# Kernel optimization log

Measured on AMD Instinct MI355X. Metric: run time of the kernel, lower is better.

## Reference

```python
import jax, jax.numpy as jnp
import numpy as np

N, EM, EW, L, S = 20000, 100000, 25000, 128, 6


def _mlp(x, W1, b1, W2, b2, g, beta):
    # Linear -> ReLU -> Linear -> LayerNorm
    h = jax.nn.relu(x @ W1 + b1) @ W2 + b2
    mu = jnp.mean(h, axis=-1, keepdims=True)
    var = jnp.mean((h - mu) ** 2, axis=-1, keepdims=True)
    return g * (h - mu) * jax.lax.rsqrt(var + 1e-5) + beta


def _scatter_mean(attr, recv, n):
    s = jax.ops.segment_sum(attr, recv, num_segments=n)
    c = jax.ops.segment_sum(jnp.ones((attr.shape[0], 1), attr.dtype), recv, num_segments=n)
    return s / jnp.maximum(c, 1.0)


def setup_inputs() -> dict:
    key = jax.random.key(0)
    ks = jax.random.split(key, 16)

    def w(k, shape, fan_in):
        return (jax.random.normal(k, shape, jnp.float32) / np.sqrt(fan_in).astype(np.float32))

    inp = {
        'x': jax.random.normal(ks[0], (N, L), jnp.float32),
        'mesh_edge_attr': jax.random.normal(ks[1], (EM, L), jnp.float32),
        'world_edge_attr': jax.random.normal(ks[2], (EW, L), jnp.float32),
        'mesh_edge_index': jax.random.randint(ks[3], (2, EM), 0, N),
        'world_edge_index': jax.random.randint(ks[4], (2, EW), 0, N),
    }
    i = 5
    for pre in ('me', 'we', 'nd'):
        inp[pre + '_W1'] = w(ks[i], (S, 3 * L, L), 3 * L); i += 1
        inp[pre + '_b1'] = jnp.zeros((S, L), jnp.float32)
        inp[pre + '_W2'] = w(ks[i], (S, L, L), L); i += 1
        inp[pre + '_b2'] = jnp.zeros((S, L), jnp.float32)
        inp[pre + '_g'] = jnp.ones((S, L), jnp.float32)
        inp[pre + '_beta'] = jnp.zeros((S, L), jnp.float32)
    return inp


def reference(x, mesh_edge_attr, world_edge_attr, mesh_edge_index, world_edge_index,
              me_W1, me_b1, me_W2, me_b2, me_g, me_beta,
              we_W1, we_b1, we_W2, we_b2, we_g, we_beta,
              nd_W1, nd_b1, nd_W2, nd_b2, nd_g, nd_beta):
    ms, mr = mesh_edge_index[0], mesh_edge_index[1]
    ws, wr = world_edge_index[0], world_edge_index[1]
    n = x.shape[0]

    def step(carry, p):
        x, mea, wea = carry
        (mW1, mb1, mW2, mb2, mg, mbe,
         wW1, wb1, wW2, wb2, wg, wbe,
         nW1, nb1, nW2, nb2, ng, nbe) = p
        # EdgeModel: gather + concat + MLP, residual into edge attrs
        mea = mea + _mlp(jnp.concatenate([x[ms], x[mr], mea], axis=-1), mW1, mb1, mW2, mb2, mg, mbe)
        wea = wea + _mlp(jnp.concatenate([x[ws], x[wr], wea], axis=-1), wW1, wb1, wW2, wb2, wg, wbe)
        # NodeModel: scatter-mean over both edge sets + concat + MLP, residual
        agg = jnp.concatenate([x, _scatter_mean(mea, mr, n), _scatter_mean(wea, wr, n)], axis=-1)
        x = x + _mlp(agg, nW1, nb1, nW2, nb2, ng, nbe)
        return (x, mea, wea), None

    params = (me_W1, me_b1, me_W2, me_b2, me_g, me_beta,
              we_W1, we_b1, we_W2, we_b2, we_g, we_beta,
              nd_W1, nd_b1, nd_W2, nd_b2, nd_g, nd_beta)
    (x, mea, wea), _ = jax.lax.scan(step, (x, mesh_edge_attr, world_edge_attr), params)
    return x, mea, wea
```

## Files before the change

### kernel.cpp

```cpp
#include <hip/hip_runtime.h>

constexpr int LDIM  = 128;
constexpr int NNODE = 20000;
constexpr int EM_N  = 100000;
constexpr int EW_N  = 25000;
constexpr int NSTEP = 6;

typedef short bf16x8 __attribute__((ext_vector_type(8)));
typedef short bf16x4 __attribute__((ext_vector_type(4)));
typedef float f32x4  __attribute__((ext_vector_type(4)));

struct MlpParams {
  const float* x;
  const float* attrIn;
  float*       attrOut;
  const int*   src;
  const int*   dst;
  float*       sum1;
  float*       sum2;
  const float* inv1;
  const float* inv2;
  const short* W1H;
  const short* W2H;
  const short* W2L;
  const float* b1;
  const float* b2;
  const float* gam;
  const float* bet;
  int nRows;
};

__device__ __forceinline__ short f2b(float f) {
  unsigned int u = __float_as_uint(f);
  u = (u + 0x7fffu + ((u >> 16) & 1u)) >> 16;
  return (short)u;
}
__device__ __forceinline__ float b2f(short s) {
  return __uint_as_float(((unsigned int)(unsigned short)s) << 16);
}
__device__ __forceinline__ bf16x4 cvt4(float4 a, float sc) {
  bf16x4 o;
  o[0] = f2b(a.x * sc); o[1] = f2b(a.y * sc);
  o[2] = f2b(a.z * sc); o[3] = f2b(a.w * sc);
  return o;
}

template<bool IS_EDGE>
__launch_bounds__(256, 2)
__global__ void mlp_kernel(MlpParams pmA, MlpParams pmB, int blocksA) {
  const bool isA = (int)blockIdx.x < blocksA;
  const MlpParams P = isA ? pmA : pmB;
  const int bid  = isA ? (int)blockIdx.x : (int)blockIdx.x - blocksA;
  const int row0 = bid * 128;

  __shared__ __align__(16) short Abuf[128][40];
  __shared__ __align__(16) short Bhi[128][40];
  __shared__ __align__(16) short Blo[128][40];
  __shared__ __align__(16) short Hbuf[128][136];
  __shared__ float b1s[128], b2s[128], gs[128], bes[128];
  __shared__ int   idxa[128], idxb[128];
  __shared__ float inv1s[128], inv2s[128];
  __shared__ float sumL[2][128], sqL[2][128];
  __shared__ float muL[128], rsL[128];

  const int t = threadIdx.x;

  if (t < 128) {
    b1s[t] = P.b1[t];
    gs[t]  = P.gam[t];
    if (IS_EDGE) {
      int r = row0 + t;
      idxa[t] = (r < P.nRows) ? P.src[r] : 0;
    } else {
      int r = min(row0 + t, P.nRows - 1);
      inv1s[t] = P.inv1[r];
    }
  } else {
    int t2 = t - 128;
    b2s[t2] = P.b2[t2];
    bes[t2] = P.bet[t2];
    if (IS_EDGE) {
      int r = row0 + t2;
      idxb[t2] = (r < P.nRows) ? P.dst[r] : 0;
    } else {
      int r = min(row0 + t2, P.nRows - 1);
      inv2s[t2] = P.inv2[r];
    }
  }
  __syncthreads();

  const int l   = t & 63;
  const int wid = t >> 6;
  const int wr  = wid >> 1, wcc = wid & 1;
  const int lr  = l & 15,  lg  = l >> 4;

  const int  srow  = t >> 1, sh = t & 1;
  const int  sgRow = row0 + srow;
  const bool sval  = sgRow < P.nRows;
  const int  sgC   = sval ? sgRow : 0;
  const float vmask = sval ? 1.f : 0.f;

  const float* base0; const float* base1; const float* base2;
  float sc1v = vmask, sc2v = vmask;
  if (IS_EDGE) {
    base0 = P.x + (size_t)idxa[srow] * LDIM + sh * 16;
    base1 = P.x + (size_t)idxb[srow] * LDIM + sh * 16;
    base2 = P.attrIn + (size_t)sgC * LDIM + sh * 16;
  } else {
    base0 = P.x    + (size_t)sgC * LDIM + sh * 16;
    base1 = P.sum1 + (size_t)sgC * LDIM + sh * 16;
    base2 = P.sum2 + (size_t)sgC * LDIM + sh * 16;
    sc1v = inv1s[srow] * vmask;
    sc2v = inv2s[srow] * vmask;
  }

  const int wrow = t >> 1, wsh = t & 1;
  const short* w1base = P.W1H + (size_t)wrow * 384 + wsh * 16;

  f32x4 acc[4][4];
#pragma unroll
  for (int i = 0; i < 4; ++i)
#pragma unroll
    for (int j = 0; j < 4; ++j) acc[i][j] = f32x4{0.f, 0.f, 0.f, 0.f};

  float4 pA0, pA1, pA2, pA3;
  bf16x8 pW0, pW1;
  {
    const float4* bp = (const float4*)base0;
    pA0 = bp[0]; pA1 = bp[1]; pA2 = bp[2]; pA3 = bp[3];
    pW0 = *(const bf16x8*)w1base;
    pW1 = *(const bf16x8*)(w1base + 8);
  }

#pragma unroll
  for (int kc = 0; kc < 12; ++kc) {
    const int seg = kc >> 2, part = kc & 3;
    if (kc > 0) __syncthreads();
    {
      const float scK = (seg == 0) ? vmask : (seg == 1) ? sc1v : sc2v;
      *(bf16x4*)&Abuf[srow][sh * 16 + 0]  = cvt4(pA0, scK);
      *(bf16x4*)&Abuf[srow][sh * 16 + 4]  = cvt4(pA1, scK);
      *(bf16x4*)&Abuf[srow][sh * 16 + 8]  = cvt4(pA2, scK);
      *(bf16x4*)&Abuf[srow][sh * 16 + 12] = cvt4(pA3, scK);
      *(bf16x8*)&Bhi[wrow][wsh * 16]     = pW0;
      *(bf16x8*)&Bhi[wrow][wsh * 16 + 8] = pW1;
      if constexpr (!IS_EDGE) {
        if (seg != 0 && sval) {
          float4 z = {0.f, 0.f, 0.f, 0.f};
          float4* zp = (float4*)((seg == 1 ? base1 : base2) + part * 32);
          zp[0] = z; zp[1] = z; zp[2] = z; zp[3] = z;
        }
      }
    }
    __syncthreads();
    if (kc < 11) {
      const int kn = kc + 1, segn = kn >> 2, partn = kn & 3;
      const float4* bp = (const float4*)((segn == 0 ? base0 : segn == 1 ? base1 : base2) + partn * 32);
      pA0 = bp[0]; pA1 = bp[1]; pA2 = bp[2]; pA3 = bp[3];
      pW0 = *(const bf16x8*)(w1base + kn * 32);
      pW1 = *(const bf16x8*)(w1base + kn * 32 + 8);
    }
    bf16x8 av[4], bh[4];
#pragma unroll
    for (int mi = 0; mi < 4; ++mi)
      av[mi] = *(const bf16x8*)&Abuf[wr * 64 + mi * 16 + lr][lg * 8];
#pragma unroll
    for (int ni = 0; ni < 4; ++ni)
      bh[ni] = *(const bf16x8*)&Bhi[wcc * 64 + ni * 16 + lr][lg * 8];
#pragma unroll
    for (int mi = 0; mi < 4; ++mi)
#pragma unroll
      for (int ni = 0; ni < 4; ++ni)
        acc[mi][ni] = __builtin_amdgcn_mfma_f32_16x16x32_bf16(av[mi], bh[ni], acc[mi][ni], 0, 0, 0);
  }

#pragma unroll
  for (int rt = 0; rt < 4; ++rt)
#pragma unroll
    for (int ct = 0; ct < 4; ++ct) {
      const int cc = wcc * 64 + ct * 16 + lr;
      const float bb = b1s[cc];
#pragma unroll
      for (int q = 0; q < 4; ++q) {
        const int rr = wr * 64 + rt * 16 + lg * 4 + q;
        Hbuf[rr][cc] = f2b(fmaxf(acc[rt][ct][q] + bb, 0.f));
      }
    }

  f32x4 acc2[4][4];
#pragma unroll
  for (int i = 0; i < 4; ++i)
#pragma unroll
    for (int j = 0; j < 4; ++j) acc2[i][j] = f32x4{0.f, 0.f, 0.f, 0.f};

  const short* w2hbase = P.W2H + (size_t)wrow * 128 + wsh * 16;
  const short* w2lbase = P.W2L + (size_t)wrow * 128 + wsh * 16;

  bf16x8 qh0, qh1, ql0, ql1;
  qh0 = *(const bf16x8*)w2hbase;
  qh1 = *(const bf16x8*)(w2hbase + 8);
  ql0 = *(const bf16x8*)w2lbase;
  ql1 = *(const bf16x8*)(w2lbase + 8);

#pragma unroll
  for (int kc = 0; kc < 4; ++kc) {
    __syncthreads();
    {
      *(bf16x8*)&Bhi[wrow][wsh * 16]     = qh0;
      *(bf16x8*)&Bhi[wrow][wsh * 16 + 8] = qh1;
      *(bf16x8*)&Blo[wrow][wsh * 16]     = ql0;
      *(bf16x8*)&Blo[wrow][wsh * 16 + 8] = ql1;
    }
    __syncthreads();
    if (kc < 3) {
      qh0 = *(const bf16x8*)(w2hbase + (kc + 1) * 32);
      qh1 = *(const bf16x8*)(w2hbase + (kc + 1) * 32 + 8);
      ql0 = *(const bf16x8*)(w2lbase + (kc + 1) * 32);
      ql1 = *(const bf16x8*)(w2lbase + (kc + 1) * 32 + 8);
    }
    bf16x8 av2[4], bh2[4], bl2[4];
#pragma unroll
    for (int rt = 0; rt < 4; ++rt)
      av2[rt] = *(const bf16x8*)&Hbuf[wr * 64 + rt * 16 + lr][kc * 32 + lg * 8];
#pragma unroll
    for (int ct = 0; ct < 4; ++ct) {
      bh2[ct] = *(const bf16x8*)&Bhi[wcc * 64 + ct * 16 + lr][lg * 8];
      bl2[ct] = *(const bf16x8*)&Blo[wcc * 64 + ct * 16 + lr][lg * 8];
    }
#pragma unroll
    for (int rt = 0; rt < 4; ++rt)
#pragma unroll
      for (int ct = 0; ct < 4; ++ct) {
        acc2[rt][ct] = __builtin_amdgcn_mfma_f32_16x16x32_bf16(av2[rt], bl2[ct], acc2[rt][ct], 0, 0, 0);
        acc2[rt][ct] = __builtin_amdgcn_mfma_f32_16x16x32_bf16(av2[rt], bh2[ct], acc2[rt][ct], 0, 0, 0);
      }
  }

  float s1[4][4], s2[4][4];
#pragma unroll
  for (int rt = 0; rt < 4; ++rt)
#pragma unroll
    for (int q = 0; q < 4; ++q) { s1[rt][q] = 0.f; s2[rt][q] = 0.f; }
#pragma unroll
  for (int rt = 0; rt < 4; ++rt)
#pragma unroll
    for (int ct = 0; ct < 4; ++ct) {
      const float bb = b2s[wcc * 64 + ct * 16 + lr];
#pragma unroll
      for (int q = 0; q < 4; ++q) {
        float v = acc2[rt][ct][q] + bb;
        acc2[rt][ct][q] = v;
        s1[rt][q] += v;
        s2[rt][q] += v * v;
      }
    }
#pragma unroll
  for (int m = 1; m < 16; m <<= 1) {
#pragma unroll
    for (int rt = 0; rt < 4; ++rt)
#pragma unroll
      for (int q = 0; q < 4; ++q) {
        s1[rt][q] += __shfl_xor(s1[rt][q], m);
        s2[rt][q] += __shfl_xor(s2[rt][q], m);
      }
  }
  __syncthreads();
  {
    const int rt = lr >> 2, q = lr & 3;
    const int rr = wr * 64 + rt * 16 + lg * 4 + q;
    sumL[wcc][rr] = s1[rt][q];
    sqL[wcc][rr]  = s2[rt][q];
  }
  __syncthreads();
  if (t < 128) {
    const float tot = sumL[0][t] + sumL[1][t];
    const float tsq = sqL[0][t] + sqL[1][t];
    const float mu  = tot * (1.0f / 128.0f);
    const float var = tsq * (1.0f / 128.0f) - mu * mu;
    muL[t] = mu;
    rsL[t] = rsqrtf(var + 1e-5f);
  }
  __syncthreads();

#pragma unroll
  for (int rt = 0; rt < 4; ++rt) {
#pragma unroll
    for (int q = 0; q < 4; ++q) {
      const int rr = wr * 64 + rt * 16 + lg * 4 + q;
      const int grow = row0 + rr;
      if (grow < P.nRows) {
        const float mu = muL[rr], rs = rsL[rr];
        const float* rin = P.attrIn + (size_t)grow * LDIM;
        float* rout = P.attrOut + (size_t)grow * LDIM;
        float* ssum = nullptr;
        if (IS_EDGE) ssum = P.sum1 + (size_t)idxb[rr] * LDIM;
#pragma unroll
        for (int ct = 0; ct < 4; ++ct) {
          const int cc = wcc * 64 + ct * 16 + lr;
          const float o = gs[cc] * (acc2[rt][ct][q] - mu) * rs + bes[cc] + rin[cc];
          rout[cc] = o;
          if (IS_EDGE) atomicAdd(ssum + cc, o);
        }
      }
    }
  }
}

__global__ void prep_weights(const float* w1a, const float* w1b, const float* w1c,
                             const float* w2a, const float* w2b, const float* w2c,
                             short* w1h, short* w2h, short* w2l) {
  int i = blockIdx.x * 256 + threadIdx.x;
  constexpr int N1 = 18 * 128 * 384;
  constexpr int N2 = 18 * 128 * 128;
  if (i < N1) {
    int g = i / (128 * 384);
    int rem = i - g * (128 * 384);
    int n = rem / 384, k = rem - n * 384;
    int m = g / 6, s = g - m * 6;
    const float* src = (m == 0) ? w1a : (m == 1) ? w1b : w1c;
    w1h[i] = f2b(src[(size_t)s * (384 * 128) + (size_t)k * 128 + n]);
  } else if (i < N1 + N2) {
    int j = i - N1;
    int g = j / (128 * 128);
    int rem = j - g * (128 * 128);
    int n = rem / 128, k = rem - n * 128;
    int m = g / 6, s = g - m * 6;
    const float* src = (m == 0) ? w2a : (m == 1) ? w2b : w2c;
    float f = src[(size_t)s * (128 * 128) + (size_t)k * 128 + n];
    short hi = f2b(f);
    w2h[j] = hi;
    w2l[j] = f2b(f - b2f(hi));
  }
}

__global__ void prep_deg(const int* mr, const int* wrcv, int* degm, int* degw) {
  int i = blockIdx.x * 256 + threadIdx.x;
  if (i < EM_N) atomicAdd(&degm[mr[i]], 1);
  else if (i < EM_N + EW_N) atomicAdd(&degw[wrcv[i - EM_N]], 1);
}

__global__ void prep_inv(const int* degm, const int* degw, float* invm, float* invw) {
  int i = blockIdx.x * 256 + threadIdx.x;
  if (i < NNODE) {
    invm[i] = 1.0f / fmaxf((float)degm[i], 1.0f);
    invw[i] = 1.0f / fmaxf((float)degw[i], 1.0f);
  }
}

extern "C" void kernel_launch(void* const* d_in, const int* in_sizes, int n_in,
                              void* d_out, int out_size, void* d_ws, size_t ws_size,
                              hipStream_t stream) {
  (void)in_sizes; (void)n_in; (void)out_size; (void)ws_size;
  const float* x_in   = (const float*)d_in[0];
  const float* mea_in = (const float*)d_in[1];
  const float* wea_in = (const float*)d_in[2];
  const int*   mei    = (const int*)d_in[3];
  const int*   wei    = (const int*)d_in[4];
  const float* W1s[3] = { (const float*)d_in[5],  (const float*)d_in[11], (const float*)d_in[17] };
  const float* B1s[3] = { (const float*)d_in[6],  (const float*)d_in[12], (const float*)d_in[18] };
  const float* W2s[3] = { (const float*)d_in[7],  (const float*)d_in[13], (const float*)d_in[19] };
  const float* B2s[3] = { (const float*)d_in[8],  (const float*)d_in[14], (const float*)d_in[20] };
  const float* Gs[3]  = { (const float*)d_in[9],  (const float*)d_in[15], (const float*)d_in[21] };
  const float* Be[3]  = { (const float*)d_in[10], (const float*)d_in[16], (const float*)d_in[22] };

  float* xo  = (float*)d_out;
  float* meo = xo  + (size_t)NNODE * LDIM;
  float* weo = meo + (size_t)EM_N * LDIM;

  float* msum = (float*)d_ws;
  float* wsum = msum + (size_t)NNODE * LDIM;
  int*   degm = (int*)(wsum + (size_t)NNODE * LDIM);
  int*   degw = degm + NNODE;
  float* invm = (float*)(degw + NNODE);
  float* invw = invm + NNODE;
  short* w1h  = (short*)(invw + NNODE);
  short* w2h  = w1h + (size_t)18 * 128 * 384;
  short* w2l  = w2h + (size_t)18 * 128 * 128;

  size_t zbytes = (size_t)2 * NNODE * LDIM * 4 + (size_t)2 * NNODE * 4;
  hipMemsetAsync(d_ws, 0, zbytes, stream);

  {
    int tot = 18 * 128 * 384 + 18 * 128 * 128;
    prep_weights<<<dim3((tot + 255) / 256), 256, 0, stream>>>(
        W1s[0], W1s[1], W1s[2], W2s[0], W2s[1], W2s[2], w1h, w2h, w2l);
  }
  prep_deg<<<dim3((EM_N + EW_N + 255) / 256), 256, 0, stream>>>(mei + EM_N, wei + EW_N, degm, degw);
  prep_inv<<<dim3((NNODE + 255) / 256), 256, 0, stream>>>(degm, degw, invm, invw);

  const int MB = (EM_N + 127) / 128;
  const int WB = (EW_N + 127) / 128;
  const int NB = (NNODE + 127) / 128;

  const float* xc = x_in;
  const float* mc = mea_in;
  const float* wc = wea_in;

  for (int s = 0; s < NSTEP; ++s) {
    MlpParams pm{}, pw{}, pn{};

    pm.x = xc; pm.attrIn = mc; pm.attrOut = meo;
    pm.src = mei; pm.dst = mei + EM_N;
    pm.sum1 = msum;
    pm.W1H = w1h + (size_t)(0 * 6 + s) * 128 * 384;
    pm.W2H = w2h + (size_t)(0 * 6 + s) * 128 * 128;
    pm.W2L = w2l + (size_t)(0 * 6 + s) * 128 * 128;
    pm.b1 = B1s[0] + s * LDIM; pm.b2 = B2s[0] + s * LDIM;
    pm.gam = Gs[0] + s * LDIM; pm.bet = Be[0] + s * LDIM;
    pm.nRows = EM_N;

    pw.x = xc; pw.attrIn = wc; pw.attrOut = weo;
    pw.src = wei; pw.dst = wei + EW_N;
    pw.sum1 = wsum;
    pw.W1H = w1h + (size_t)(1 * 6 + s) * 128 * 384;
    pw.W2H = w2h + (size_t)(1 * 6 + s) * 128 * 128;
    pw.W2L = w2l + (size_t)(1 * 6 + s) * 128 * 128;
    pw.b1 = B1s[1] + s * LDIM; pw.b2 = B2s[1] + s * LDIM;
    pw.gam = Gs[1] + s * LDIM; pw.bet = Be[1] + s * LDIM;
    pw.nRows = EW_N;

    mlp_kernel<true><<<dim3(MB + WB), 256, 0, stream>>>(pm, pw, MB);

    pn.x = xc; pn.attrIn = xc; pn.attrOut = xo;
    pn.sum1 = msum; pn.sum2 = wsum; pn.inv1 = invm; pn.inv2 = invw;
    pn.W1H = w1h + (size_t)(2 * 6 + s) * 128 * 384;
    pn.W2H = w2h + (size_t)(2 * 6 + s) * 128 * 128;
    pn.W2L = w2l + (size_t)(2 * 6 + s) * 128 * 128;
    pn.b1 = B1s[2] + s * LDIM; pn.b2 = B2s[2] + s * LDIM;
    pn.gam = Gs[2] + s * LDIM; pn.bet = Be[2] + s * LDIM;
    pn.nRows = NNODE;

    mlp_kernel<false><<<dim3(NB), 256, 0, stream>>>(pn, pn, NB);

    xc = xo; mc = meo; wc = weo;
  }
}
```

Before: 886.0 us.

## Drop split-bf16 W2 correction and alias A-tile into H buffer for occupancy

Removes the low-order bf16 correction term for the second-layer weights, halving the second GEMM's MFMA count and its weight traffic. The A staging tile now reuses the H buffer's shared memory, which together with the removed Blo buffer cuts LDS usage so launch bounds can ask for 3 blocks per CU. A barrier is added before H is written so the aliasing stays safe. The trade-off is lower precision in the W2 product, which may drift over the six steps.

New measurement: 919.6 us. 1.04x slower.

```diff
diff --git a/kernel.cpp b/kernel.cpp
--- a/kernel.cpp
+++ b/kernel.cpp
@@ -22,7 +22,6 @@
   const float* inv2;
   const short* W1H;
   const short* W2H;
-  const short* W2L;
   const float* b1;
   const float* b2;
   const float* gam;
@@ -46,22 +45,22 @@
 }
 
 template<bool IS_EDGE>
-__launch_bounds__(256, 2)
+__launch_bounds__(256, 3)
 __global__ void mlp_kernel(MlpParams pmA, MlpParams pmB, int blocksA) {
   const bool isA = (int)blockIdx.x < blocksA;
   const MlpParams P = isA ? pmA : pmB;
   const int bid  = isA ? (int)blockIdx.x : (int)blockIdx.x - blocksA;
   const int row0 = bid * 128;
 
-  __shared__ __align__(16) short Abuf[128][40];
+  __shared__ __align__(16) short Hbuf[128][136];
   __shared__ __align__(16) short Bhi[128][40];
-  __shared__ __align__(16) short Blo[128][40];
-  __shared__ __align__(16) short Hbuf[128][136];
   __shared__ float b1s[128], b2s[128], gs[128], bes[128];
   __shared__ int   idxa[128], idxb[128];
   __shared__ float inv1s[128], inv2s[128];
   __shared__ float sumL[2][128], sqL[2][128];
   __shared__ float muL[128], rsL[128];
+
+  short (*Abuf)[40] = (short (*)[40])(&Hbuf[0][0]);
 
   const int t = threadIdx.x;
 
@@ -174,6 +173,8 @@
         acc[mi][ni] = __builtin_amdgcn_mfma_f32_16x16x32_bf16(av[mi], bh[ni], acc[mi][ni], 0, 0, 0);
   }
 
+  __syncthreads();
+
 #pragma unroll
   for (int rt = 0; rt < 4; ++rt)
 #pragma unroll
@@ -193,47 +194,34 @@
 #pragma unroll
     for (int j = 0; j < 4; ++j) acc2[i][j] = f32x4{0.f, 0.f, 0.f, 0.f};
 
-  const short* w2hbase = P.W2H + (size_t)wrow * 128 + wsh * 16;
-  const short* w2lbase = P.W2L + (size_t)wrow * 128 + wsh * 16;
-
-  bf16x8 qh0, qh1, ql0, ql1;
-  qh0 = *(const bf16x8*)w2hbase;
-  qh1 = *(const bf16x8*)(w2hbase + 8);
-  ql0 = *(const bf16x8*)w2lbase;
-  ql1 = *(const bf16x8*)(w2lbase + 8);
+  const short* w2base = P.W2H + (size_t)wrow * 128 + wsh * 16;
+  bf16x8 q0 = *(const bf16x8*)w2base;
+  bf16x8 q1 = *(const bf16x8*)(w2base + 8);
 
 #pragma unroll
   for (int kc = 0; kc < 4; ++kc) {
     __syncthreads();
     {
-      *(bf16x8*)&Bhi[wrow][wsh * 16]     = qh0;
-      *(bf16x8*)&Bhi[wrow][wsh * 16 + 8] = qh1;
-      *(bf16x8*)&Blo[wrow][wsh * 16]     = ql0;
-      *(bf16x8*)&Blo[wrow][wsh * 16 + 8] = ql1;
+      *(bf16x8*)&Bhi[wrow][wsh * 16]     = q0;
+      *(bf16x8*)&Bhi[wrow][wsh * 16 + 8] = q1;
     }
     __syncthreads();
     if (kc < 3) {
-      qh0 = *(const bf16x8*)(w2hbase + (kc + 1) * 32);
-      qh1 = *(const bf16x8*)(w2hbase + (kc + 1) * 32 + 8);
-      ql0 = *(const bf16x8*)(w2lbase + (kc + 1) * 32);
-      ql1 = *(const bf16x8*)(w2lbase + (kc + 1) * 32 + 8);
-    }
-    bf16x8 av2[4], bh2[4], bl2[4];
+      q0 = *(const bf16x8*)(w2base + (kc + 1) * 32);
+      q1 = *(const bf16x8*)(w2base + (kc + 1) * 32 + 8);
+    }
+    bf16x8 av2[4], bh2[4];
 #pragma unroll
     for (int rt = 0; rt < 4; ++rt)
       av2[rt] = *(const bf16x8*)&Hbuf[wr * 64 + rt * 16 + lr][kc * 32 + lg * 8];
 #pragma unroll
-    for (int ct = 0; ct < 4; ++ct) {
+    for (int ct = 0; ct < 4; ++ct)
       bh2[ct] = *(const bf16x8*)&Bhi[wcc * 64 + ct * 16 + lr][lg * 8];
-      bl2[ct] = *(const bf16x8*)&Blo[wcc * 64 + ct * 16 + lr][lg * 8];
-    }
 #pragma unroll
     for (int rt = 0; rt < 4; ++rt)
 #pragma unroll
-      for (int ct = 0; ct < 4; ++ct) {
-        acc2[rt][ct] = __builtin_amdgcn_mfma_f32_16x16x32_bf16(av2[rt], bl2[ct], acc2[rt][ct], 0, 0, 0);
+      for (int ct = 0; ct < 4; ++ct)
         acc2[rt][ct] = __builtin_amdgcn_mfma_f32_16x16x32_bf16(av2[rt], bh2[ct], acc2[rt][ct], 0, 0, 0);
-      }
   }
 
   float s1[4][4], s2[4][4];
@@ -308,7 +296,7 @@
 
 __global__ void prep_weights(const float* w1a, const float* w1b, const float* w1c,
                              const float* w2a, const float* w2b, const float* w2c,
-                             short* w1h, short* w2h, short* w2l) {
+                             short* w1h, short* w2h) {
   int i = blockIdx.x * 256 + threadIdx.x;
   constexpr int N1 = 18 * 128 * 384;
   constexpr int N2 = 18 * 128 * 128;
@@ -326,10 +314,7 @@
     int n = rem / 128, k = rem - n * 128;
     int m = g / 6, s = g - m * 6;
     const float* src = (m == 0) ? w2a : (m == 1) ? w2b : w2c;
-    float f = src[(size_t)s * (128 * 128) + (size_t)k * 128 + n];
-    short hi = f2b(f);
-    w2h[j] = hi;
-    w2l[j] = f2b(f - b2f(hi));
+    w2h[j] = f2b(src[(size_t)s * (128 * 128) + (size_t)k * 128 + n]);
   }
 }
 
@@ -375,7 +360,6 @@
   float* invw = invm + NNODE;
   short* w1h  = (short*)(invw + NNODE);
   short* w2h  = w1h + (size_t)18 * 128 * 384;
-  short* w2l  = w2h + (size_t)18 * 128 * 128;
 
   size_t zbytes = (size_t)2 * NNODE * LDIM * 4 + (size_t)2 * NNODE * 4;
   hipMemsetAsync(d_ws, 0, zbytes, stream);
@@ -383,7 +367,7 @@
   {
     int tot = 18 * 128 * 384 + 18 * 128 * 128;
     prep_weights<<<dim3((tot + 255) / 256), 256, 0, stream>>>(
-        W1s[0], W1s[1], W1s[2], W2s[0], W2s[1], W2s[2], w1h, w2h, w2l);
+        W1s[0], W1s[1], W1s[2], W2s[0], W2s[1], W2s[2], w1h, w2h);
   }
   prep_deg<<<dim3((EM_N + EW_N + 255) / 256), 256, 0, stream>>>(mei + EM_N, wei + EW_N, degm, degw);
   prep_inv<<<dim3((NNODE + 255) / 256), 256, 0, stream>>>(degm, degw, invm, invw);
@@ -404,7 +388,6 @@
     pm.sum1 = msum;
     pm.W1H = w1h + (size_t)(0 * 6 + s) * 128 * 384;
     pm.W2H = w2h + (size_t)(0 * 6 + s) * 128 * 128;
-    pm.W2L = w2l + (size_t)(0 * 6 + s) * 128 * 128;
     pm.b1 = B1s[0] + s * LDIM; pm.b2 = B2s[0] + s * LDIM;
     pm.gam = Gs[0] + s * LDIM; pm.bet = Be[0] + s * LDIM;
     pm.nRows = EM_N;
@@ -414,7 +397,6 @@
     pw.sum1 = wsum;
     pw.W1H = w1h + (size_t)(1 * 6 + s) * 128 * 384;
     pw.W2H = w2h + (size_t)(1 * 6 + s) * 128 * 128;
-    pw.W2L = w2l + (size_t)(1 * 6 + s) * 128 * 128;
     pw.b1 = B1s[1] + s * LDIM; pw.b2 = B2s[1] + s * LDIM;
     pw.gam = Gs[1] + s * LDIM; pw.bet = Be[1] + s * LDIM;
     pw.nRows = EW_N;
@@ -425,7 +407,6 @@
     pn.sum1 = msum; pn.sum2 = wsum; pn.inv1 = invm; pn.inv2 = invw;
     pn.W1H = w1h + (size_t)(2 * 6 + s) * 128 * 384;
     pn.W2H = w2h + (size_t)(2 * 6 + s) * 128 * 128;
-    pn.W2L = w2l + (size_t)(2 * 6 + s) * 128 * 128;
     pn.b1 = B1s[2] + s * LDIM; pn.b2 = B2s[2] + s * LDIM;
     pn.gam = Gs[2] + s * LDIM; pn.bet = Be[2] + s * LDIM;
     pn.nRows = NNODE;
```

## Replace atomic scatter-mean with CSR gather aggregation in node kernel

Applied to the files above, without the earlier changes.

Edge kernels no longer atomically add their outputs into per-node sum buffers. A CSR index (offsets plus edge lists per receiver) is built once at setup, and the node kernel gathers and averages incoming edge features directly while staging its A tiles. This removes the float atomics, the large sum-buffer memset and the zeroing writes. The cost is that node-kernel loads become irregular, serialized per-row loops that can no longer be prefetched, and the float summation order changes.

New measurement: 1.033 ms. +16.6%, slower.

```diff
diff --git a/kernel.cpp b/kernel.cpp
--- a/kernel.cpp
+++ b/kernel.cpp
@@ -16,10 +16,12 @@
   float*       attrOut;
   const int*   src;
   const int*   dst;
-  float*       sum1;
-  float*       sum2;
-  const float* inv1;
-  const float* inv2;
+  const float* gsrc1;
+  const float* gsrc2;
+  const int*   off1;
+  const int*   csr1;
+  const int*   off2;
+  const int*   csr2;
   const short* W1H;
   const short* W2H;
   const short* W2L;
@@ -44,10 +46,12 @@
   o[2] = f2b(a.z * sc); o[3] = f2b(a.w * sc);
   return o;
 }
-
-template<bool IS_EDGE>
+__device__ __forceinline__ void add4(float4& a, const float4 b) {
+  a.x += b.x; a.y += b.y; a.z += b.z; a.w += b.w;
+}
+
 __launch_bounds__(256, 2)
-__global__ void mlp_kernel(MlpParams pmA, MlpParams pmB, int blocksA) {
+__global__ void edge_kernel(MlpParams pmA, MlpParams pmB, int blocksA) {
   const bool isA = (int)blockIdx.x < blocksA;
   const MlpParams P = isA ? pmA : pmB;
   const int bid  = isA ? (int)blockIdx.x : (int)blockIdx.x - blocksA;
@@ -59,7 +63,6 @@
   __shared__ __align__(16) short Hbuf[128][136];
   __shared__ float b1s[128], b2s[128], gs[128], bes[128];
   __shared__ int   idxa[128], idxb[128];
-  __shared__ float inv1s[128], inv2s[128];
   __shared__ float sumL[2][128], sqL[2][128];
   __shared__ float muL[128], rsL[128];
 
@@ -68,24 +71,14 @@
   if (t < 128) {
     b1s[t] = P.b1[t];
     gs[t]  = P.gam[t];
-    if (IS_EDGE) {
-      int r = row0 + t;
-      idxa[t] = (r < P.nRows) ? P.src[r] : 0;
-    } else {
-      int r = min(row0 + t, P.nRows - 1);
-      inv1s[t] = P.inv1[r];
-    }
+    int r = row0 + t;
+    idxa[t] = (r < P.nRows) ? P.src[r] : 0;
   } else {
     int t2 = t - 128;
     b2s[t2] = P.b2[t2];
     bes[t2] = P.bet[t2];
-    if (IS_EDGE) {
-      int r = row0 + t2;
-      idxb[t2] = (r < P.nRows) ? P.dst[r] : 0;
-    } else {
-      int r = min(row0 + t2, P.nRows - 1);
-      inv2s[t2] = P.inv2[r];
-    }
+    int r = row0 + t2;
+    idxb[t2] = (r < P.nRows) ? P.dst[r] : 0;
   }
   __syncthreads();
 
@@ -100,19 +93,9 @@
   const int  sgC   = sval ? sgRow : 0;
   const float vmask = sval ? 1.f : 0.f;
 
-  const float* base0; const float* base1; const float* base2;
-  float sc1v = vmask, sc2v = vmask;
-  if (IS_EDGE) {
-    base0 = P.x + (size_t)idxa[srow] * LDIM + sh * 16;
-    base1 = P.x + (size_t)idxb[srow] * LDIM + sh * 16;
-    base2 = P.attrIn + (size_t)sgC * LDIM + sh * 16;
-  } else {
-    base0 = P.x    + (size_t)sgC * LDIM + sh * 16;
-    base1 = P.sum1 + (size_t)sgC * LDIM + sh * 16;
-    base2 = P.sum2 + (size_t)sgC * LDIM + sh * 16;
-    sc1v = inv1s[srow] * vmask;
-    sc2v = inv2s[srow] * vmask;
-  }
+  const float* base0 = P.x + (size_t)idxa[srow] * LDIM + sh * 16;
+  const float* base1 = P.x + (size_t)idxb[srow] * LDIM + sh * 16;
+  const float* base2 = P.attrIn + (size_t)sgC * LDIM + sh * 16;
 
   const int wrow = t >> 1, wsh = t & 1;
   const short* w1base = P.W1H + (size_t)wrow * 384 + wsh * 16;
@@ -134,23 +117,14 @@
 
 #pragma unroll
   for (int kc = 0; kc < 12; ++kc) {
-    const int seg = kc >> 2, part = kc & 3;
     if (kc > 0) __syncthreads();
     {
-      const float scK = (seg == 0) ? vmask : (seg == 1) ? sc1v : sc2v;
-      *(bf16x4*)&Abuf[srow][sh * 16 + 0]  = cvt4(pA0, scK);
-      *(bf16x4*)&Abuf[srow][sh * 16 + 4]  = cvt4(pA1, scK);
-      *(bf16x4*)&Abuf[srow][sh * 16 + 8]  = cvt4(pA2, scK);
-      *(bf16x4*)&Abuf[srow][sh * 16 + 12] = cvt4(pA3, scK);
+      *(bf16x4*)&Abuf[srow][sh * 16 + 0]  = cvt4(pA0, vmask);
+      *(bf16x4*)&Abuf[srow][sh * 16 + 4]  = cvt4(pA1, vmask);
+      *(bf16x4*)&Abuf[srow][sh * 16 + 8]  = cvt4(pA2, vmask);
+      *(bf16x4*)&Abuf[srow][sh * 16 + 12] = cvt4(pA3, vmask);
       *(bf16x8*)&Bhi[wrow][wsh * 16]     = pW0;
       *(bf16x8*)&Bhi[wrow][wsh * 16 + 8] = pW1;
-      if constexpr (!IS_EDGE) {
-        if (seg != 0 && sval) {
-          float4 z = {0.f, 0.f, 0.f, 0.f};
-          float4* zp = (float4*)((seg == 1 ? base1 : base2) + part * 32);
-          zp[0] = z; zp[1] = z; zp[2] = z; zp[3] = z;
-        }
-      }
     }
     __syncthreads();
     if (kc < 11) {
@@ -196,11 +170,10 @@
   const short* w2hbase = P.W2H + (size_t)wrow * 128 + wsh * 16;
   const short* w2lbase = P.W2L + (size_t)wrow * 128 + wsh * 16;
 
-  bf16x8 qh0, qh1, ql0, ql1;
-  qh0 = *(const bf16x8*)w2hbase;
-  qh1 = *(const bf16x8*)(w2hbase + 8);
-  ql0 = *(const bf16x8*)w2lbase;
-  ql1 = *(const bf16x8*)(w2lbase + 8);
+  bf16x8 qh0 = *(const bf16x8*)w2hbase;
+  bf16x8 qh1 = *(const bf16x8*)(w2hbase + 8);
+  bf16x8 ql0 = *(const bf16x8*)w2lbase;
+  bf16x8 ql1 = *(const bf16x8*)(w2lbase + 8);
 
 #pragma unroll
   for (int kc = 0; kc < 4; ++kc) {
@@ -292,14 +265,220 @@
         const float mu = muL[rr], rs = rsL[rr];
         const float* rin = P.attrIn + (size_t)grow * LDIM;
         float* rout = P.attrOut + (size_t)grow * LDIM;
-        float* ssum = nullptr;
-        if (IS_EDGE) ssum = P.sum1 + (size_t)idxb[rr] * LDIM;
 #pragma unroll
         for (int ct = 0; ct < 4; ++ct) {
           const int cc = wcc * 64 + ct * 16 + lr;
-          const float o = gs[cc] * (acc2[rt][ct][q] - mu) * rs + bes[cc] + rin[cc];
-          rout[cc] = o;
-          if (IS_EDGE) atomicAdd(ssum + cc, o);
+          rout[cc] = gs[cc] * (acc2[rt][ct][q] - mu) * rs + bes[cc] + rin[cc];
+        }
+      }
+    }
+  }
+}
+
+__launch_bounds__(256, 2)
+__global__ void node_kernel(MlpParams P) {
+  const int bid  = (int)blockIdx.x;
+  const int row0 = bid * 128;
+
+  __shared__ __align__(16) short Abuf[128][40];
+  __shared__ __align__(16) short Bhi[128][40];
+  __shared__ __align__(16) short Blo[128][40];
+  __shared__ __align__(16) short Hbuf[128][136];
+  __shared__ float b1s[128], b2s[128], gs[128], bes[128];
+  __shared__ float sumL[2][128], sqL[2][128];
+  __shared__ float muL[128], rsL[128];
+
+  const int t = threadIdx.x;
+  if (t < 128) { b1s[t] = P.b1[t]; gs[t] = P.gam[t]; }
+  else         { b2s[t - 128] = P.b2[t - 128]; bes[t - 128] = P.bet[t - 128]; }
+
+  const int l   = t & 63;
+  const int wid = t >> 6;
+  const int wr  = wid >> 1, wcc = wid & 1;
+  const int lr  = l & 15,  lg  = l >> 4;
+
+  const int  srow  = t >> 1, sh = t & 1;
+  const int  sgRow = row0 + srow;
+  const bool sval  = sgRow < P.nRows;
+
+  const int wrow = t >> 1, wsh = t & 1;
+  const short* w1base = P.W1H + (size_t)wrow * 384 + wsh * 16;
+
+  f32x4 acc[4][4];
+#pragma unroll
+  for (int i = 0; i < 4; ++i)
+#pragma unroll
+    for (int j = 0; j < 4; ++j) acc[i][j] = f32x4{0.f, 0.f, 0.f, 0.f};
+
+  __syncthreads();
+
+#pragma unroll
+  for (int kc = 0; kc < 12; ++kc) {
+    const int seg = kc >> 2, part = kc & 3;
+    if (kc > 0) __syncthreads();
+    {
+      float4 s0{0,0,0,0}, s1{0,0,0,0}, s2{0,0,0,0}, s3{0,0,0,0};
+      float sc = 1.f;
+      if (seg == 0) {
+        if (sval) {
+          const float4* p = (const float4*)(P.x + (size_t)sgRow * LDIM + part * 32 + sh * 16);
+          s0 = p[0]; s1 = p[1]; s2 = p[2]; s3 = p[3];
+        }
+      } else {
+        const int* off = (seg == 1) ? P.off1 : P.off2;
+        const int* csr = (seg == 1) ? P.csr1 : P.csr2;
+        const float* src = (seg == 1) ? P.gsrc1 : P.gsrc2;
+        int beg = 0, end = 0;
+        if (sval) { beg = off[sgRow]; end = off[sgRow + 1]; }
+        for (int i = beg; i < end; ++i) {
+          const float4* p = (const float4*)(src + (size_t)csr[i] * LDIM + part * 32 + sh * 16);
+          add4(s0, p[0]); add4(s1, p[1]); add4(s2, p[2]); add4(s3, p[3]);
+        }
+        sc = 1.0f / (float)max(end - beg, 1);
+      }
+      *(bf16x4*)&Abuf[srow][sh * 16 + 0]  = cvt4(s0, sc);
+      *(bf16x4*)&Abuf[srow][sh * 16 + 4]  = cvt4(s1, sc);
+      *(bf16x4*)&Abuf[srow][sh * 16 + 8]  = cvt4(s2, sc);
+      *(bf16x4*)&Abuf[srow][sh * 16 + 12] = cvt4(s3, sc);
+      const short* wsrc = w1base + kc * 32;
+      *(bf16x8*)&Bhi[wrow][wsh * 16]     = *(const bf16x8*)wsrc;
+      *(bf16x8*)&Bhi[wrow][wsh * 16 + 8] = *(const bf16x8*)(wsrc + 8);
+    }
+    __syncthreads();
+    bf16x8 av[4], bh[4];
+#pragma unroll
+    for (int mi = 0; mi < 4; ++mi)
+      av[mi] = *(const bf16x8*)&Abuf[wr * 64 + mi * 16 + lr][lg * 8];
+#pragma unroll
+    for (int ni = 0; ni < 4; ++ni)
+      bh[ni] = *(const bf16x8*)&Bhi[wcc * 64 + ni * 16 + lr][lg * 8];
+#pragma unroll
+    for (int mi = 0; mi < 4; ++mi)
+#pragma unroll
+      for (int ni = 0; ni < 4; ++ni)
+        acc[mi][ni] = __builtin_amdgcn_mfma_f32_16x16x32_bf16(av[mi], bh[ni], acc[mi][ni], 0, 0, 0);
+  }
+
+#pragma unroll
+  for (int rt = 0; rt < 4; ++rt)
+#pragma unroll
+    for (int ct = 0; ct < 4; ++ct) {
+      const int cc = wcc * 64 + ct * 16 + lr;
+      const float bb = b1s[cc];
+#pragma unroll
+      for (int q = 0; q < 4; ++q) {
+        const int rr = wr * 64 + rt * 16 + lg * 4 + q;
+        Hbuf[rr][cc] = f2b(fmaxf(acc[rt][ct][q] + bb, 0.f));
+      }
+    }
+
+  f32x4 acc2[4][4];
+#pragma unroll
+  for (int i = 0; i < 4; ++i)
+#pragma unroll
+    for (int j = 0; j < 4; ++j) acc2[i][j] = f32x4{0.f, 0.f, 0.f, 0.f};
+
+  const short* w2hbase = P.W2H + (size_t)wrow * 128 + wsh * 16;
+  const short* w2lbase = P.W2L + (size_t)wrow * 128 + wsh * 16;
+  bf16x8 qh0 = *(const bf16x8*)w2hbase;
+  bf16x8 qh1 = *(const bf16x8*)(w2hbase + 8);
+  bf16x8 ql0 = *(const bf16x8*)w2lbase;
+  bf16x8 ql1 = *(const bf16x8*)(w2lbase + 8);
+
+#pragma unroll
+  for (int kc = 0; kc < 4; ++kc) {
+    __syncthreads();
+    {
+      *(bf16x8*)&Bhi[wrow][wsh * 16]     = qh0;
+      *(bf16x8*)&Bhi[wrow][wsh * 16 + 8] = qh1;
+      *(bf16x8*)&Blo[wrow][wsh * 16]     = ql0;
+      *(bf16x8*)&Blo[wrow][wsh * 16 + 8] = ql1;
+    }
+    __syncthreads();
+    if (kc < 3) {
+      qh0 = *(const bf16x8*)(w2hbase + (kc + 1) * 32);
+      qh1 = *(const bf16x8*)(w2hbase + (kc + 1) * 32 + 8);
+      ql0 = *(const bf16x8*)(w2lbase + (kc + 1) * 32);
+      ql1 = *(const bf16x8*)(w2lbase + (kc + 1) * 32 + 8);
+    }
+    bf16x8 av2[4], bh2[4], bl2[4];
+#pragma unroll
+    for (int rt = 0; rt < 4; ++rt)
+      av2[rt] = *(const bf16x8*)&Hbuf[wr * 64 + rt * 16 + lr][kc * 32 + lg * 8];
+#pragma unroll
+    for (int ct = 0; ct < 4; ++ct) {
+      bh2[ct] = *(const bf16x8*)&Bhi[wcc * 64 + ct * 16 + lr][lg * 8];
+      bl2[ct] = *(const bf16x8*)&Blo[wcc * 64 + ct * 16 + lr][lg * 8];
+    }
+#pragma unroll
+    for (int rt = 0; rt < 4; ++rt)
+#pragma unroll
+      for (int ct = 0; ct < 4; ++ct) {
+        acc2[rt][ct] = __builtin_amdgcn_mfma_f32_16x16x32_bf16(av2[rt], bl2[ct], acc2[rt][ct], 0, 0, 0);
+        acc2[rt][ct] = __builtin_amdgcn_mfma_f32_16x16x32_bf16(av2[rt], bh2[ct], acc2[rt][ct], 0, 0, 0);
+      }
+  }
+
+  float s1[4][4], s2[4][4];
+#pragma unroll
+  for (int rt = 0; rt < 4; ++rt)
+#pragma unroll
+    for (int q = 0; q < 4; ++q) { s1[rt][q] = 0.f; s2[rt][q] = 0.f; }
+#pragma unroll
+  for (int rt = 0; rt < 4; ++rt)
+#pragma unroll
+    for (int ct = 0; ct < 4; ++ct) {
+      const float bb = b2s[wcc * 64 + ct * 16 + lr];
+#pragma unroll
+      for (int q = 0; q < 4; ++q) {
+        float v = acc2[rt][ct][q] + bb;
+        acc2[rt][ct][q] = v;
+        s1[rt][q] += v;
+        s2[rt][q] += v * v;
+      }
+    }
+#pragma unroll
+  for (int m = 1; m < 16; m <<= 1) {
+#pragma unroll
+    for (int rt = 0; rt < 4; ++rt)
+#pragma unroll
+      for (int q = 0; q < 4; ++q) {
+        s1[rt][q] += __shfl_xor(s1[rt][q], m);
+        s2[rt][q] += __shfl_xor(s2[rt][q], m);
+      }
+  }
+  __syncthreads();
+  {
+    const int rt = lr >> 2, q = lr & 3;
+    const int rr = wr * 64 + rt * 16 + lg * 4 + q;
+    sumL[wcc][rr] = s1[rt][q];
+    sqL[wcc][rr]  = s2[rt][q];
+  }
+  __syncthreads();
+  if (t < 128) {
+    const float tot = sumL[0][t] + sumL[1][t];
+    const float tsq = sqL[0][t] + sqL[1][t];
+    const float mu  = tot * (1.0f / 128.0f);
+    const float var = tsq * (1.0f / 128.0f) - mu * mu;
+    muL[t] = mu;
+    rsL[t] = rsqrtf(var + 1e-5f);
+  }
+  __syncthreads();
+
+#pragma unroll
+  for (int rt = 0; rt < 4; ++rt) {
+#pragma unroll
+    for (int q = 0; q < 4; ++q) {
+      const int rr = wr * 64 + rt * 16 + lg * 4 + q;
+      const int grow = row0 + rr;
+      if (grow < P.nRows) {
+        const float mu = muL[rr], rs = rsL[rr];
+        const float* rin = P.attrIn + (size_t)grow * LDIM;
+        float* rout = P.attrOut + (size_t)grow * LDIM;
+#pragma unroll
+        for (int ct = 0; ct < 4; ++ct) {
+          const int cc = wcc * 64 + ct * 16 + lr;
+          rout[cc] = gs[cc] * (acc2[rt][ct][q] - mu) * rs + bes[cc] + rin[cc];
         }
       }
     }
@@ -339,11 +518,50 @@
   else if (i < EM_N + EW_N) atomicAdd(&degw[wrcv[i - EM_N]], 1);
 }
 
-__global__ void prep_inv(const int* degm, const int* degw, float* invm, float* invw) {
+__global__ void prep_scan(const int* degm, const int* degw, int* moff, int* woff) {
+  __shared__ int part[256];
+  const int t = threadIdx.x;
+  constexpr int NPT = (NNODE + 255) / 256;
+#pragma unroll 1
+  for (int pass = 0; pass < 2; ++pass) {
+    const int* deg = pass == 0 ? degm : degw;
+    int* off = pass == 0 ? moff : woff;
+    int s = 0;
+    for (int i = 0; i < NPT; ++i) {
+      int n = t * NPT + i;
+      if (n < NNODE) s += deg[n];
+    }
+    part[t] = s;
+    __syncthreads();
+    for (int d = 1; d < 256; d <<= 1) {
+      int v = (t >= d) ? part[t - d] : 0;
+      __syncthreads();
+      part[t] += v;
+      __syncthreads();
+    }
+    int base = (t == 0) ? 0 : part[t - 1];
+    for (int i = 0; i < NPT; ++i) {
+      int n = t * NPT + i;
+      if (n < NNODE) { off[n] = base; base += deg[n]; }
+    }
+    if (t == 255) off[NNODE] = base;
+    __syncthreads();
+  }
+}
+
+__global__ void prep_fill(const int* mr, const int* wrcv,
+                          const int* moff, const int* woff,
+                          int* mcur, int* wcur, int* mcsr, int* wcsr) {
   int i = blockIdx.x * 256 + threadIdx.x;
-  if (i < NNODE) {
-    invm[i] = 1.0f / fmaxf((float)degm[i], 1.0f);
-    invw[i] = 1.0f / fmaxf((float)degw[i], 1.0f);
+  if (i < EM_N) {
+    int d = mr[i];
+    int pos = moff[d] + atomicAdd(&mcur[d], 1);
+    mcsr[pos] = i;
+  } else if (i < EM_N + EW_N) {
+    int j = i - EM_N;
+    int d = wrcv[j];
+    int pos = woff[d] + atomicAdd(&wcur[d], 1);
+    wcsr[pos] = j;
   }
 }
 
@@ -367,18 +585,19 @@
   float* meo = xo  + (size_t)NNODE * LDIM;
   float* weo = meo + (size_t)EM_N * LDIM;
 
-  float* msum = (float*)d_ws;
-  float* wsum = msum + (size_t)NNODE * LDIM;
-  int*   degm = (int*)(wsum + (size_t)NNODE * LDIM);
+  int*   degm = (int*)d_ws;
   int*   degw = degm + NNODE;
-  float* invm = (float*)(degw + NNODE);
-  float* invw = invm + NNODE;
-  short* w1h  = (short*)(invw + NNODE);
+  int*   mcur = degw + NNODE;
+  int*   wcur = mcur + NNODE;
+  int*   moff = wcur + NNODE;
+  int*   woff = moff + (NNODE + 1);
+  int*   mcsr = woff + (NNODE + 1);
+  int*   wcsr = mcsr + EM_N;
+  short* w1h  = (short*)(wcsr + EW_N);
   short* w2h  = w1h + (size_t)18 * 128 * 384;
   short* w2l  = w2h + (size_t)18 * 128 * 128;
 
-  size_t zbytes = (size_t)2 * NNODE * LDIM * 4 + (size_t)2 * NNODE * 4;
-  hipMemsetAsync(d_ws, 0, zbytes, stream);
+  hipMemsetAsync(d_ws, 0, (size_t)4 * NNODE * 4, stream);
 
   {
     int tot = 18 * 128 * 384 + 18 * 128 * 128;
@@ -386,7 +605,9 @@
         W1s[0], W1s[1], W1s[2], W2s[0], W2s[1], W2s[2], w1h, w2h, w2l);
   }
   prep_deg<<<dim3((EM_N + EW_N + 255) / 256), 256, 0, stream>>>(mei + EM_N, wei + EW_N, degm, degw);
-  prep_inv<<<dim3((NNODE + 255) / 256), 256, 0, stream>>>(degm, degw, invm, invw);
+  prep_scan<<<dim3(1), 256, 0, stream>>>(degm, degw, moff, woff);
+  prep_fill<<<dim3((EM_N + EW_N + 255) / 256), 256, 0, stream>>>(
+      mei + EM_N, wei + EW_N, moff, woff, mcur, wcur, mcsr, wcsr);
 
   const int MB = (EM_N + 127) / 128;
   const int WB = (EW_N + 127) / 128;
@@ -401,7 +622,6 @@
 
     pm.x = xc; pm.attrIn = mc; pm.attrOut = meo;
     pm.src = mei; pm.dst = mei + EM_N;
-    pm.sum1 = msum;
     pm.W1H = w1h + (size_t)(0 * 6 + s) * 128 * 384;
     pm.W2H = w2h + (size_t)(0 * 6 + s) * 128 * 128;
     pm.W2L = w2l + (size_t)(0 * 6 + s) * 128 * 128;
@@ -411,7 +631,6 @@
 
     pw.x = xc; pw.attrIn = wc; pw.attrOut = weo;
     pw.src = wei; pw.dst = wei + EW_N;
-    pw.sum1 = wsum;
     pw.W1H = w1h + (size_t)(1 * 6 + s) * 128 * 384;
     pw.W2H = w2h + (size_t)(1 * 6 + s) * 128 * 128;
     pw.W2L = w2l + (size_t)(1 * 6 + s) * 128 * 128;
@@ -419,10 +638,12 @@
     pw.gam = Gs[1] + s * LDIM; pw.bet = Be[1] + s * LDIM;
     pw.nRows = EW_N;
 
-    mlp_kernel<true><<<dim3(MB + WB), 256, 0, stream>>>(pm, pw, MB);
+    edge_kernel<<<dim3(MB + WB), 256, 0, stream>>>(pm, pw, MB);
 
     pn.x = xc; pn.attrIn = xc; pn.attrOut = xo;
-    pn.sum1 = msum; pn.sum2 = wsum; pn.inv1 = invm; pn.inv2 = invw;
+    pn.gsrc1 = meo; pn.gsrc2 = weo;
+    pn.off1 = moff; pn.csr1 = mcsr;
+    pn.off2 = woff; pn.csr2 = wcsr;
     pn.W1H = w1h + (size_t)(2 * 6 + s) * 128 * 384;
     pn.W2H = w2h + (size_t)(2 * 6 + s) * 128 * 128;
     pn.W2L = w2l + (size_t)(2 * 6 + s) * 128 * 128;
@@ -430,7 +651,7 @@
     pn.gam = Gs[2] + s * LDIM; pn.bet = Be[2] + s * LDIM;
     pn.nRows = NNODE;
 
-    mlp_kernel<false><<<dim3(NB), 256, 0, stream>>>(pn, pn, NB);
+    node_kernel<<<dim3(NB), 256, 0, stream>>>(pn);
 
     xc = xo; mc = meo; wc = weo;
   }
```
